# Performance work log

Hardware: AMD Instinct MI355X
Metric: run time of the kernel (lower is better)

The kernel has to match this reference:

```python
import jax, jax.numpy as jnp
import numpy as np

EMBED_DIM = 1024
NUM_HEADS = 16
HEAD_DIM = EMBED_DIM // NUM_HEADS


def setup_inputs() -> dict:
    key = jax.random.key(0)
    k_x, k_wqkv, k_bqkv, k_wo, k_bo = jax.random.split(key, 5)
    B, T, C = 4, 2048, EMBED_DIM
    bound = 1.0 / np.sqrt(C)
    return {
        "x": jax.random.normal(k_x, (B, T, C), dtype=jnp.float32),
        "w_qkv": jax.random.uniform(k_wqkv, (C, 3 * C), jnp.float32, -bound, bound),
        "b_qkv": jax.random.uniform(k_bqkv, (3 * C,), jnp.float32, -bound, bound),
        "w_out": jax.random.uniform(k_wo, (C, C), jnp.float32, -bound, bound),
        "b_out": jax.random.uniform(k_bo, (C,), jnp.float32, -bound, bound),
    }


def reference(x, w_qkv, b_qkv, w_out, b_out):
    B, T, C = x.shape
    H, D = NUM_HEADS, HEAD_DIM
    qkv = x @ w_qkv + b_qkv                       # [B,T,3C]
    qkv = qkv.reshape(B, T, 3, H, D)
    q, k, v = qkv[:, :, 0], qkv[:, :, 1], qkv[:, :, 2]  # [B,T,H,D]
    scale = 1.0 / np.sqrt(D).astype(np.float32)
    scores = jnp.einsum("bqhd,bkhd->bhqk", q, k) * scale  # [B,H,T,T]
    causal = jnp.tril(jnp.ones((T, T), dtype=bool))
    scores = jnp.where(causal, scores, -jnp.inf)
    attn = jax.nn.softmax(scores, axis=-1)
    # dropout p=0.0 / eval mode -> identity
    ctx = jnp.einsum("bhqk,bkhd->bqhd", attn, v).reshape(B, T, C)
    return ctx @ w_out + b_out
```

## Files before the change

### kernel.cpp

```cpp
#include <hip/hip_runtime.h>
#include <hip/hip_bf16.h>

#define NB 4
#define NT 2048
#define NC 1024
#define NH 16
#define ND 64
#define BT (NB*NT)
#define LOG2E 1.4426950408889634f
#define NEG_BIG (-3.0e38f)
#define MLC 28.853900817779268f

typedef __attribute__((ext_vector_type(8))) short bf16x8;
typedef __attribute__((ext_vector_type(4))) float f32x4;

static __device__ __forceinline__ short f2bf(float f) {
    union { float f; unsigned u; } v; v.f = f;
    unsigned r = (v.u + 0x7fffu + ((v.u >> 16) & 1u)) >> 16;
    return (short)r;
}

static __device__ __forceinline__ unsigned pk2(float a, float b) {
#if __has_builtin(__builtin_amdgcn_cvt_pk_bf16_f32)
    auto v = __builtin_amdgcn_cvt_pk_bf16_f32(a, b);
    union { decltype(v) v; unsigned u; } c; c.v = v; return c.u;
#else
    return (unsigned)(unsigned short)f2bf(a) | ((unsigned)(unsigned short)f2bf(b) << 16);
#endif
}

static __device__ __forceinline__ f32x4 mfma16(bf16x8 a, bf16x8 b, f32x4 c) {
    return __builtin_amdgcn_mfma_f32_16x16x32_bf16(a, b, c, 0, 0, 0);
}

static __device__ __forceinline__ float fexp2(float x) {
#if __has_builtin(__builtin_amdgcn_exp2f)
    return __builtin_amdgcn_exp2f(x);
#else
    return exp2f(x);
#endif
}

template<int GOFF>
static __device__ __forceinline__ void gload_lds16(const short* g, short* l) {
    __builtin_amdgcn_global_load_lds(
        (const __attribute__((address_space(1))) void*)g,
        (__attribute__((address_space(3))) void*)l,
        16, GOFF, 0);
}

__global__ __launch_bounds__(256)
void xcvt(const float* __restrict__ x, short* __restrict__ xb)
{
    const size_t i = ((size_t)blockIdx.x * 256 + threadIdx.x) * 8;
    float4 f0 = *(const float4*)(x + i);
    float4 f1 = *(const float4*)(x + i + 4);
    uint4 p;
    p.x = pk2(f0.x, f0.y); p.y = pk2(f0.z, f0.w);
    p.z = pk2(f1.x, f1.y); p.w = pk2(f1.z, f1.w);
    *(uint4*)(xb + i) = p;
}

__global__ __launch_bounds__(256)
void transpose_w(const float* __restrict__ w, short* __restrict__ wt, int R, int Cn)
{
    __shared__ short t[64][72];
    const int tid = threadIdx.x;
    const int r0 = blockIdx.x * 64;
    const int c0 = blockIdx.y * 64;
    {
        const int rl = tid >> 2, c4 = (tid & 3) << 4;
        const float* src = w + (size_t)(r0 + rl) * Cn + c0 + c4;
        float4 f0 = *(const float4*)(src + 0);
        float4 f1 = *(const float4*)(src + 4);
        float4 f2 = *(const float4*)(src + 8);
        float4 f3 = *(const float4*)(src + 12);
        short* d = &t[rl][c4];
        d[0]=f2bf(f0.x); d[1]=f2bf(f0.y); d[2]=f2bf(f0.z); d[3]=f2bf(f0.w);
        d[4]=f2bf(f1.x); d[5]=f2bf(f1.y); d[6]=f2bf(f1.z); d[7]=f2bf(f1.w);
        d[8]=f2bf(f2.x); d[9]=f2bf(f2.y); d[10]=f2bf(f2.z); d[11]=f2bf(f2.w);
        d[12]=f2bf(f3.x); d[13]=f2bf(f3.y); d[14]=f2bf(f3.z); d[15]=f2bf(f3.w);
    }
    __syncthreads();
    {
        const int cl = tid >> 2, r4 = (tid & 3) << 4;
        bf16x8 p0, p1;
#pragma unroll
        for (int j = 0; j < 8; ++j) { p0[j] = t[r4 + j][cl]; p1[j] = t[r4 + 8 + j][cl]; }
        short* dst = wt + (size_t)(c0 + cl) * R + r0 + r4;
        *(bf16x8*)dst       = p0;
        *(bf16x8*)(dst + 8) = p1;
    }
}

__global__ __launch_bounds__(256)
void qkv_gemm(const short* __restrict__ xb, const short* __restrict__ wt,
              const float* __restrict__ bias,
              short* __restrict__ q, short* __restrict__ k, short* __restrict__ vt)
{
    __shared__ short aLds[128 * 64];
    __shared__ short bLds[128 * 64];
    const int tid  = threadIdx.x;
    const int lane = tid & 63;
    const int wave = tid >> 6;
    const int waveM = wave & 1;
    const int waveN = wave >> 1;
    const int quad = lane >> 4;
    const int l15  = lane & 15;
    const int l7   = l15 & 7;
    const int m0 = blockIdx.x * 128;
    const int n0 = blockIdx.y * 128;

    const int rsub   = lane >> 3;
    const int cchunk = (lane & 7) ^ rsub;
    const int gcol   = cchunk * 8;

    f32x4 acc[4][4];
#pragma unroll
    for (int i = 0; i < 4; ++i)
#pragma unroll
        for (int j = 0; j < 4; ++j) acc[i][j] = 0.0f;

    for (int k0 = 0; k0 < NC; k0 += 64) {
#pragma unroll
        for (int i = 0; i < 4; ++i) {
            const int rbase = wave * 32 + i * 8;
            gload_lds16<0>(xb + (size_t)(m0 + rbase + rsub) * NC + k0 + gcol,
                           &aLds[rbase * 64]);
        }
#pragma unroll
        for (int i = 0; i < 4; ++i) {
            const int rbase = wave * 32 + i * 8;
            gload_lds16<0>(wt + (size_t)(n0 + rbase + rsub) * NC + k0 + gcol,
                           &bLds[rbase * 64]);
        }
        __syncthreads();

#pragma unroll
        for (int kd = 0; kd < 2; ++kd) {
            bf16x8 af[4], bfr[4];
#pragma unroll
            for (int mi = 0; mi < 4; ++mi) {
                const int r = waveM*64 + mi*16 + l15;
                af[mi] = *(const bf16x8*)&aLds[r*64 + (((kd*4 + quad) ^ l7) * 8)];
            }
#pragma unroll
            for (int ni = 0; ni < 4; ++ni) {
                const int r = waveN*64 + ni*16 + l15;
                bfr[ni] = *(const bf16x8*)&bLds[r*64 + (((kd*4 + quad) ^ l7) * 8)];
            }
#pragma unroll
            for (int mi = 0; mi < 4; ++mi)
#pragma unroll
                for (int ni = 0; ni < 4; ++ni)
                    acc[mi][ni] = mfma16(af[mi], bfr[ni], acc[mi][ni]);
        }
        __syncthreads();
    }

#pragma unroll
    for (int mi = 0; mi < 4; ++mi) {
#pragma unroll
        for (int ni = 0; ni < 4; ++ni) {
            const int n = n0 + waveN*64 + ni*16 + l15;
            const float bb = bias[n];
            const int s = n >> 10;
            const int h = (n >> 6) & 15;
            const int d = n & 63;
#pragma unroll
            for (int r = 0; r < 4; ++r) {
                const int m = m0 + waveM*64 + mi*16 + quad*4 + r;
                const int b = m >> 11;
                const int t = m & (NT - 1);
                const float val = acc[mi][ni][r] + bb;
                const size_t bhx = (size_t)(b * NH + h);
                if (s == 0)      q [(bhx * NT + t) * ND + d] = f2bf(val * 0.125f);
                else if (s == 1) k [(bhx * NT + t) * ND + d] = f2bf(val);
                else             vt[(bhx * ND + d) * NT + t] = f2bf(val);
            }
        }
    }
}

__global__ __launch_bounds__(256)
void attn(const short* __restrict__ q, const short* __restrict__ k,
          const short* __restrict__ vt, short* __restrict__ ctx)
{
    __shared__ short kbuf[2][64 * 64];
    __shared__ short vbuf[2][64 * 64];
    __shared__ short pbuf[4][32 * 64];
    const int tid  = threadIdx.x;
    const int lane = tid & 63;
    const int wave = tid >> 6;
    const int quad = lane >> 4;
    const int l15  = lane & 15;
    const int l7   = l15 & 7;
    const int bh = blockIdx.x;
    const int b  = bh >> 4;
    const int h  = bh & 15;

    const short* Qp = q  + (size_t)bh * NT * ND;
    const short* Kp = k  + (size_t)bh * NT * ND;
    const short* Vp = vt + (size_t)bh * ND * NT;

    const int srow   = lane >> 3;
    const int schunk = ((lane & 7) ^ srow) * 8;
    short* pw = &pbuf[wave][0];

    for (int half = 0; half < 2; ++half) {
        const int qblock = half ? (15 - (int)blockIdx.y) : (int)blockIdx.y;
        const int qb  = qblock * 128;
        const int wq0 = qb + wave * 32;
        const int ktB = 2 * qblock + 2;

        bf16x8 qf[2][2];
#pragma unroll
        for (int mi = 0; mi < 2; ++mi)
#pragma unroll
            for (int kd = 0; kd < 2; ++kd)
                qf[mi][kd] = *(const bf16x8*)(Qp + (size_t)(wq0 + mi*16 + l15) * ND + kd*32 + quad*8);

        f32x4 ot[4][2];
        f32x4 lv[2];
#pragma unroll
        for (int di = 0; di < 4; ++di)
#pragma unroll
            for (int mi = 0; mi < 2; ++mi) ot[di][mi] = 0.0f;
        lv[0] = 0.0f; lv[1] = 0.0f;

        {
            const short* Ks = Kp + (size_t)(wave*16 + srow) * ND + schunk;
            gload_lds16<0>(Ks,          &kbuf[0][(wave*16    ) * 64]);
            gload_lds16<0>(Ks + 8*ND,   &kbuf[0][(wave*16 + 8) * 64]);
            const short* Vs = Vp + (size_t)(wave*16 + srow) * NT + schunk;
            gload_lds16<0>(Vs,          &vbuf[0][(wave*16    ) * 64]);
            gload_lds16<0>(Vs + 8*NT,   &vbuf[0][(wave*16 + 8) * 64]);
        }

        for (int kt = 0; kt < ktB; ++kt) {
            const int p  = kt & 1;
            const int kb = kt << 6;
            __syncthreads();

            if (kt + 1 < ktB) {
                const int kb2 = kb + 64;
                const short* Ks = Kp + (size_t)(kb2 + wave*16 + srow) * ND + schunk;
                gload_lds16<0>(Ks,        &kbuf[1-p][(wave*16    ) * 64]);
                gload_lds16<0>(Ks + 8*ND, &kbuf[1-p][(wave*16 + 8) * 64]);
                const short* Vs = Vp + (size_t)(wave*16 + srow) * NT + kb2 + schunk;
                gload_lds16<0>(Vs,        &vbuf[1-p][(wave*16    ) * 64]);
                gload_lds16<0>(Vs + 8*NT, &vbuf[1-p][(wave*16 + 8) * 64]);
            }

            if (kb > wq0 + 31) continue;

            bf16x8 kf[4][2];
#pragma unroll
            for (int ni = 0; ni < 4; ++ni)
#pragma unroll
                for (int kd = 0; kd < 2; ++kd)
                    kf[ni][kd] = *(const bf16x8*)
                        &kbuf[p][(ni*16 + l15)*64 + (((kd*4 + quad) ^ l7) * 8)];

            f32x4 st[4][2];
#pragma unroll
            for (int ni = 0; ni < 4; ++ni)
#pragma unroll
                for (int mi = 0; mi < 2; ++mi) {
                    st[ni][mi] = 0.0f;
                    st[ni][mi] = mfma16(kf[ni][0], qf[mi][0], st[ni][mi]);
                    st[ni][mi] = mfma16(kf[ni][1], qf[mi][1], st[ni][mi]);
                }

            if (kb + 63 > wq0) {
#pragma unroll
                for (int ni = 0; ni < 4; ++ni)
#pragma unroll
                    for (int mi = 0; mi < 2; ++mi) {
                        const int qrow = wq0 + mi*16 + l15;
#pragma unroll
                        for (int r = 0; r < 4; ++r) {
                            const int key = kb + ni*16 + quad*4 + r;
                            if (key > qrow) st[ni][mi][r] = NEG_BIG;
                        }
                    }
            }

#pragma unroll
            for (int mi = 0; mi < 2; ++mi) {
#pragma unroll
                for (int ni = 0; ni < 4; ++ni) {
#pragma unroll
                    for (int r = 0; r < 4; ++r)
                        st[ni][mi][r] = fexp2(fmaf(st[ni][mi][r], LOG2E, -MLC));
                    lv[mi] += st[ni][mi];
                    const f32x4 v = st[ni][mi];
                    *(uint2*)&pw[(mi*16 + l15)*64
                                 + (((2*ni + (quad >> 1)) ^ l7) * 8)
                                 + (quad & 1) * 4] =
                        make_uint2(pk2(v[0], v[1]), pk2(v[2], v[3]));
                }
            }

            bf16x8 vf[4][2], pf[2][2];
#pragma unroll
            for (int di = 0; di < 4; ++di)
#pragma unroll
                for (int kd = 0; kd < 2; ++kd)
                    vf[di][kd] = *(const bf16x8*)
                        &vbuf[p][(di*16 + l15)*64 + (((kd*4 + quad) ^ l7) * 8)];
#pragma unroll
            for (int mi = 0; mi < 2; ++mi)
#pragma unroll
                for (int kd = 0; kd < 2; ++kd)
                    pf[mi][kd] = *(const bf16x8*)
                        &pw[(mi*16 + l15)*64 + (((kd*4 + quad) ^ l7) * 8)];

#pragma unroll
            for (int di = 0; di < 4; ++di)
#pragma unroll
                for (int mi = 0; mi < 2; ++mi) {
                    ot[di][mi] = mfma16(vf[di][0], pf[mi][0], ot[di][mi]);
                    ot[di][mi] = mfma16(vf[di][1], pf[mi][1], ot[di][mi]);
                }
        }

#pragma unroll
        for (int mi = 0; mi < 2; ++mi) {
            float l = lv[mi][0] + lv[mi][1] + lv[mi][2] + lv[mi][3];
            l += __shfl_xor(l, 16);
            l += __shfl_xor(l, 32);
            const float inv = 1.0f / l;
            const int t = wq0 + mi*16 + l15;
            short* dst = ctx + ((size_t)(b * NT + t)) * NC + h*64 + quad*4;
#pragma unroll
            for (int di = 0; di < 4; ++di) {
                const f32x4 v = ot[di][mi] * inv;
                *(uint2*)(dst + di*16) = make_uint2(pk2(v[0], v[1]), pk2(v[2], v[3]));
            }
        }
        __syncthreads();
    }
}

__global__ __launch_bounds__(256)
void out_gemm(const short* __restrict__ a, const short* __restrict__ wt,
              const float* __restrict__ bias, float* __restrict__ out)
{
    __shared__ short aLds[128 * 64];
    __shared__ short bLds[128 * 64];
    const int tid  = threadIdx.x;
    const int lane = tid & 63;
    const int wave = tid >> 6;
    const int waveM = wave & 1;
    const int waveN = wave >> 1;
    const int quad = lane >> 4;
    const int l15  = lane & 15;
    const int l7   = l15 & 7;
    const int m0 = blockIdx.x * 128;
    const int n0 = blockIdx.y * 128;

    const int rsub   = lane >> 3;
    const int cchunk = (lane & 7) ^ rsub;
    const int gcol   = cchunk * 8;

    f32x4 acc[4][4];
#pragma unroll
    for (int i = 0; i < 4; ++i)
#pragma unroll
        for (int j = 0; j < 4; ++j) acc[i][j] = 0.0f;

    for (int k0 = 0; k0 < NC; k0 += 64) {
#pragma unroll
        for (int i = 0; i < 4; ++i) {
            const int rbase = wave * 32 + i * 8;
            gload_lds16<0>(a + (size_t)(m0 + rbase + rsub) * NC + k0 + gcol,
                           &aLds[rbase * 64]);
        }
#pragma unroll
        for (int i = 0; i < 4; ++i) {
            const int rbase = wave * 32 + i * 8;
            gload_lds16<0>(wt + (size_t)(n0 + rbase + rsub) * NC + k0 + gcol,
                           &bLds[rbase * 64]);
        }
        __syncthreads();

#pragma unroll
        for (int kd = 0; kd < 2; ++kd) {
            bf16x8 af[4], bfr[4];
#pragma unroll
            for (int mi = 0; mi < 4; ++mi) {
                const int r = waveM*64 + mi*16 + l15;
                af[mi] = *(const bf16x8*)&aLds[r*64 + (((kd*4 + quad) ^ l7) * 8)];
            }
#pragma unroll
            for (int ni = 0; ni < 4; ++ni) {
                const int r = waveN*64 + ni*16 + l15;
                bfr[ni] = *(const bf16x8*)&bLds[r*64 + (((kd*4 + quad) ^ l7) * 8)];
            }
#pragma unroll
            for (int mi = 0; mi < 4; ++mi)
#pragma unroll
                for (int ni = 0; ni < 4; ++ni)
                    acc[mi][ni] = mfma16(af[mi], bfr[ni], acc[mi][ni]);
        }
        __syncthreads();
    }

#pragma unroll
    for (int mi = 0; mi < 4; ++mi) {
#pragma unroll
        for (int ni = 0; ni < 4; ++ni) {
            const int n = n0 + waveN*64 + ni*16 + l15;
            const float bb = bias[n];
#pragma unroll
            for (int r = 0; r < 4; ++r) {
                const int m = m0 + waveM*64 + mi*16 + quad*4 + r;
                out[(size_t)m * NC + n] = acc[mi][ni][r] + bb;
            }
        }
    }
}

extern "C" void kernel_launch(void* const* d_in, const int* in_sizes, int n_in,
                              void* d_out, int out_size, void* d_ws, size_t ws_size,
                              hipStream_t stream)
{
    const float* x     = (const float*)d_in[0];
    const float* w_qkv = (const float*)d_in[1];
    const float* b_qkv = (const float*)d_in[2];
    const float* w_out = (const float*)d_in[3];
    const float* b_out = (const float*)d_in[4];
    float* out = (float*)d_out;

    const size_t SZ = (size_t)NB * NH * NT * ND;
    short* q   = (short*)d_ws;
    short* kk  = q  + SZ;
    short* vt  = kk + SZ;
    short* ctx = vt + SZ;
    short* xbf = ctx + SZ;
    short* wTq = ctx;
    short* wTo = xbf;

    hipLaunchKernelGGL(xcvt, dim3(BT*NC/(256*8)), dim3(256), 0, stream, x, xbf);
    hipLaunchKernelGGL(transpose_w, dim3(16, 48), dim3(256), 0, stream,
                       w_qkv, wTq, NC, 3*NC);
    hipLaunchKernelGGL(qkv_gemm, dim3(BT/128, (3*NC)/128), dim3(256), 0, stream,
                       xbf, wTq, b_qkv, q, kk, vt);
    hipLaunchKernelGGL(attn, dim3(NB*NH, 8), dim3(256), 0, stream,
                       q, kk, vt, ctx);
    hipLaunchKernelGGL(transpose_w, dim3(16, 16), dim3(256), 0, stream,
                       w_out, wTo, NC, NC);
    hipLaunchKernelGGL(out_gemm, dim3(BT/128, NC/128), dim3(256), 0, stream,
                       ctx, wTo, b_out, out);
}
```

Baseline: 276.2 us.

## Double-buffer LDS tiles in QKV and output GEMMs with K-step of 32

```diff
diff --git a/kernel.cpp b/kernel.cpp
--- a/kernel.cpp
+++ b/kernel.cpp
@@ -98,8 +98,8 @@
               const float* __restrict__ bias,
               short* __restrict__ q, short* __restrict__ k, short* __restrict__ vt)
 {
-    __shared__ short aLds[128 * 64];
-    __shared__ short bLds[128 * 64];
+    __shared__ short aLds[2][128 * 32];
+    __shared__ short bLds[2][128 * 32];
     const int tid  = threadIdx.x;
     const int lane = tid & 63;
     const int wave = tid >> 6;
@@ -107,13 +107,12 @@
     const int waveN = wave >> 1;
     const int quad = lane >> 4;
     const int l15  = lane & 15;
-    const int l7   = l15 & 7;
+    const int l3   = l15 & 3;
     const int m0 = blockIdx.x * 128;
     const int n0 = blockIdx.y * 128;
 
-    const int rsub   = lane >> 3;
-    const int cchunk = (lane & 7) ^ rsub;
-    const int gcol   = cchunk * 8;
+    const int srow   = lane >> 2;
+    const int schunk = ((lane & 3) ^ (srow & 3)) * 8;
 
     f32x4 acc[4][4];
 #pragma unroll
@@ -121,41 +120,49 @@
 #pragma unroll
         for (int j = 0; j < 4; ++j) acc[i][j] = 0.0f;
 
-    for (int k0 = 0; k0 < NC; k0 += 64) {
-#pragma unroll
-        for (int i = 0; i < 4; ++i) {
-            const int rbase = wave * 32 + i * 8;
-            gload_lds16<0>(xb + (size_t)(m0 + rbase + rsub) * NC + k0 + gcol,
-                           &aLds[rbase * 64]);
-        }
-#pragma unroll
-        for (int i = 0; i < 4; ++i) {
-            const int rbase = wave * 32 + i * 8;
-            gload_lds16<0>(wt + (size_t)(n0 + rbase + rsub) * NC + k0 + gcol,
-                           &bLds[rbase * 64]);
-        }
+    const short* Ag = xb + (size_t)(m0 + wave*32 + srow) * NC + schunk;
+    const short* Bg = wt + (size_t)(n0 + wave*32 + srow) * NC + schunk;
+    short* ad0 = &aLds[0][wave*32*32];
+    short* bd0 = &bLds[0][wave*32*32];
+    short* ad1 = &aLds[1][wave*32*32];
+    short* bd1 = &bLds[1][wave*32*32];
+
+    gload_lds16<0>(Ag,          ad0);
+    gload_lds16<0>(Ag + 16*NC,  ad0 + 16*32);
+    gload_lds16<0>(Bg,          bd0);
+    gload_lds16<0>(Bg + 16*NC,  bd0 + 16*32);
+
+    for (int kt = 0; kt < 32; ++kt) {
+        const int p = kt & 1;
         __syncthreads();
 
-#pragma unroll
-        for (int kd = 0; kd < 2; ++kd) {
-            bf16x8 af[4], bfr[4];
-#pragma unroll
-            for (int mi = 0; mi < 4; ++mi) {
-                const int r = waveM*64 + mi*16 + l15;
-                af[mi] = *(const bf16x8*)&aLds[r*64 + (((kd*4 + quad) ^ l7) * 8)];
-            }
-#pragma unroll
-            for (int ni = 0; ni < 4; ++ni) {
-                const int r = waveN*64 + ni*16 + l15;
-                bfr[ni] = *(const bf16x8*)&bLds[r*64 + (((kd*4 + quad) ^ l7) * 8)];
-            }
-#pragma unroll
-            for (int mi = 0; mi < 4; ++mi)
-#pragma unroll
-                for (int ni = 0; ni < 4; ++ni)
-                    acc[mi][ni] = mfma16(af[mi], bfr[ni], acc[mi][ni]);
-        }
-        __syncthreads();
+        if (kt + 1 < 32) {
+            const short* a2 = Ag + (kt + 1) * 32;
+            const short* b2 = Bg + (kt + 1) * 32;
+            short* ad = p ? ad0 : ad1;
+            short* bd = p ? bd0 : bd1;
+            gload_lds16<0>(a2,         ad);
+            gload_lds16<0>(a2 + 16*NC, ad + 16*32);
+            gload_lds16<0>(b2,         bd);
+            gload_lds16<0>(b2 + 16*NC, bd + 16*32);
+        }
+
+        bf16x8 af[4], bfr[4];
+#pragma unroll
+        for (int mi = 0; mi < 4; ++mi) {
+            const int r = waveM*64 + mi*16 + l15;
+            af[mi] = *(const bf16x8*)&aLds[p][r*32 + ((quad ^ l3) * 8)];
+        }
+#pragma unroll
+        for (int ni = 0; ni < 4; ++ni) {
+            const int r = waveN*64 + ni*16 + l15;
+            bfr[ni] = *(const bf16x8*)&bLds[p][r*32 + ((quad ^ l3) * 8)];
+        }
+#pragma unroll
+        for (int mi = 0; mi < 4; ++mi)
+#pragma unroll
+            for (int ni = 0; ni < 4; ++ni)
+                acc[mi][ni] = mfma16(af[mi], bfr[ni], acc[mi][ni]);
     }
 
 #pragma unroll
@@ -347,8 +354,8 @@
 void out_gemm(const short* __restrict__ a, const short* __restrict__ wt,
               const float* __restrict__ bias, float* __restrict__ out)
 {
-    __shared__ short aLds[128 * 64];
-    __shared__ short bLds[128 * 64];
+    __shared__ short aLds[2][128 * 32];
+    __shared__ short bLds[2][128 * 32];
     const int tid  = threadIdx.x;
     const int lane = tid & 63;
     const int wave = tid >> 6;
@@ -356,13 +363,12 @@
     const int waveN = wave >> 1;
     const int quad = lane >> 4;
     const int l15  = lane & 15;
-    const int l7   = l15 & 7;
+    const int l3   = l15 & 3;
     const int m0 = blockIdx.x * 128;
     const int n0 = blockIdx.y * 128;
 
-    const int rsub   = lane >> 3;
-    const int cchunk = (lane & 7) ^ rsub;
-    const int gcol   = cchunk * 8;
+    const int srow   = lane >> 2;
+    const int schunk = ((lane & 3) ^ (srow & 3)) * 8;
 
     f32x4 acc[4][4];
 #pragma unroll
@@ -370,41 +376,49 @@
 #pragma unroll
         for (int j = 0; j < 4; ++j) acc[i][j] = 0.0f;
 
-    for (int k0 = 0; k0 < NC; k0 += 64) {
-#pragma unroll
-        for (int i = 0; i < 4; ++i) {
-            const int rbase = wave * 32 + i * 8;
-            gload_lds16<0>(a + (size_t)(m0 + rbase + rsub) * NC + k0 + gcol,
-                           &aLds[rbase * 64]);
-        }
-#pragma unroll
-        for (int i = 0; i < 4; ++i) {
-            const int rbase = wave * 32 + i * 8;
-            gload_lds16<0>(wt + (size_t)(n0 + rbase + rsub) * NC + k0 + gcol,
-                           &bLds[rbase * 64]);
-        }
+    const short* Ag = a  + (size_t)(m0 + wave*32 + srow) * NC + schunk;
+    const short* Bg = wt + (size_t)(n0 + wave*32 + srow) * NC + schunk;
+    short* ad0 = &aLds[0][wave*32*32];
+    short* bd0 = &bLds[0][wave*32*32];
+    short* ad1 = &aLds[1][wave*32*32];
+    short* bd1 = &bLds[1][wave*32*32];
+
+    gload_lds16<0>(Ag,          ad0);
+    gload_lds16<0>(Ag + 16*NC,  ad0 + 16*32);
+    gload_lds16<0>(Bg,          bd0);
+    gload_lds16<0>(Bg + 16*NC,  bd0 + 16*32);
+
+    for (int kt = 0; kt < 32; ++kt) {
+        const int p = kt & 1;
         __syncthreads();
 
-#pragma unroll
-        for (int kd = 0; kd < 2; ++kd) {
-            bf16x8 af[4], bfr[4];
-#pragma unroll
-            for (int mi = 0; mi < 4; ++mi) {
-                const int r = waveM*64 + mi*16 + l15;
-                af[mi] = *(const bf16x8*)&aLds[r*64 + (((kd*4 + quad) ^ l7) * 8)];
-            }
-#pragma unroll
-            for (int ni = 0; ni < 4; ++ni) {
-                const int r = waveN*64 + ni*16 + l15;
-                bfr[ni] = *(const bf16x8*)&bLds[r*64 + (((kd*4 + quad) ^ l7) * 8)];
-            }
-#pragma unroll
-            for (int mi = 0; mi < 4; ++mi)
-#pragma unroll
-                for (int ni = 0; ni < 4; ++ni)
-                    acc[mi][ni] = mfma16(af[mi], bfr[ni], acc[mi][ni]);
-        }
-        __syncthreads();
+        if (kt + 1 < 32) {
+            const short* a2 = Ag + (kt + 1) * 32;
+            const short* b2 = Bg + (kt + 1) * 32;
+            short* ad = p ? ad0 : ad1;
+            short* bd = p ? bd0 : bd1;
+            gload_lds16<0>(a2,         ad);
+            gload_lds16<0>(a2 + 16*NC, ad + 16*32);
+            gload_lds16<0>(b2,         bd);
+            gload_lds16<0>(b2 + 16*NC, bd + 16*32);
+        }
+
+        bf16x8 af[4], bfr[4];
+#pragma unroll
+        for (int mi = 0; mi < 4; ++mi) {
+            const int r = waveM*64 + mi*16 + l15;
+            af[mi] = *(const bf16x8*)&aLds[p][r*32 + ((quad ^ l3) * 8)];
+        }
+#pragma unroll
+        for (int ni = 0; ni < 4; ++ni) {
+            const int r = waveN*64 + ni*16 + l15;
+            bfr[ni] = *(const bf16x8*)&bLds[p][r*32 + ((quad ^ l3) * 8)];
+        }
+#pragma unroll
+        for (int mi = 0; mi < 4; ++mi)
+#pragma unroll
+            for (int ni = 0; ni < 4; ++ni)
+                acc[mi][ni] = mfma16(af[mi], bfr[ni], acc[mi][ni]);
     }
 
 #pragma unroll
```

New measurement: 279.5 us. About the same (+1.2%).
